# Kernel tuning notes

Measured on AMD Instinct MI355X. Metric: run time of the kernel, lower is better.

The kernel has to match this reference:

```python
import jax, jax.numpy as jnp
import numpy as np

B, CIN, H, W = 8, 256, 96, 96
EMB1, EMB2 = 256, 128
NCLS, NEG, NLAY = 80, 3, 3
SIGMA, BETA, NEG_SCOPE = 0.5, 0.3, 2.0


def setup_inputs() -> dict:
    key = jax.random.key(0)
    ks = jax.random.split(key, 8)
    s = 0.01
    return {
        "x": jax.random.normal(ks[0], (B, CIN, H, W), jnp.float32),
        "conv1_w": jax.random.normal(ks[1], (EMB1, CIN, 3, 3), jnp.float32) * s,
        "conv1_b": jnp.zeros((EMB1,), jnp.float32),
        "bn_gamma": jnp.ones((EMB1,), jnp.float32),
        "bn_beta": jnp.zeros((EMB1,), jnp.float32),
        "bn_mean": jnp.zeros((EMB1,), jnp.float32),
        "bn_var": jnp.ones((EMB1,), jnp.float32),
        "conv2_w": jax.random.normal(ks[2], (EMB2, EMB1, 3, 3), jnp.float32) * s,
        "conv2_b": jnp.zeros((EMB2,), jnp.float32),
        "rep_w": jax.random.normal(ks[3], (NCLS * EMB2, 1), jnp.float32) * s,
        "rep_b": jax.random.normal(ks[4], (NCLS * EMB2,), jnp.float32) * s,
        "neg_w": jax.random.normal(ks[5], (NEG, NLAY, EMB2, EMB2), jnp.float32) * s,
        "neg_b": jnp.zeros((NEG, NLAY, EMB2), jnp.float32),
    }


def _conv3(x, w, b):
    # 3x3, stride 1, padding 1 (SAME)
    y = jax.lax.conv_general_dilated(
        x, w, window_strides=(1, 1), padding="SAME",
        dimension_numbers=("NCHW", "OIHW", "NCHW"))
    return y + b[None, :, None, None]


def _l2norm(v, axis):
    return v / jnp.maximum(jnp.linalg.norm(v, axis=axis, keepdims=True), 1e-12)


def reference(x, conv1_w, conv1_b, bn_gamma, bn_beta, bn_mean, bn_var,
              conv2_w, conv2_b, rep_w, rep_b, neg_w, neg_b):
    # --- emb_module: Conv-BN-Conv, then L2 normalize channels ---
    h = _conv3(x, conv1_w, conv1_b)
    scale = bn_gamma / jnp.sqrt(bn_var + 1e-5)
    h = (h - bn_mean[None, :, None, None]) * scale[None, :, None, None] + bn_beta[None, :, None, None]
    emb = _conv3(h, conv2_w, conv2_b)          # [B, E, H, W]
    emb = _l2norm(emb, axis=1)

    # --- positive prototypes: rep_fc(1.0) -> [C, 1, E], normalized ---
    reps = (rep_w[:, 0] + rep_b).reshape(NCLS, 1, EMB2)
    reps = _l2norm(reps, axis=2)               # [C, 1, E]
    r = reps[:, 0]                              # [C, E]

    # --- negative prototypes: 3 MPCs (Linear-ReLU-Linear-ReLU-Linear) ---
    def mpc(Ws, bs):                            # Ws [NLAY,E,E], bs [NLAY,E]
        hh = r
        for i in range(NLAY):
            hh = hh @ Ws[i].T + bs[i]
            if i < NLAY - 1:
                hh = jax.nn.relu(hh)
        return hh                               # [C, E]
    reps_neg = jax.vmap(mpc)(neg_w, neg_b)      # [NEG, C, E]
    reps_neg = jnp.transpose(reps_neg, (1, 0, 2))  # [C, NEG, E]
    reps_neg = _l2norm(reps_neg, axis=2)

    # --- L2 distances; both sides unit-norm so ||e-r||^2 = 2 - 2 e.r ---
    dot = jnp.einsum("behw,cme->bcmhw", emb, reps)       # [B,C,1,H,W]
    distances = jnp.sqrt(jnp.maximum(2.0 - 2.0 * dot, 0.0))
    dot_n = jnp.einsum("behw,cme->bcmhw", emb, reps_neg)  # [B,C,NEG,H,W]
    distances_neg = jnp.sqrt(jnp.maximum(2.0 - 2.0 * dot_n, 0.0))

    inv2s2 = 1.0 / (2.0 * SIGMA ** 2)
    probs_neg = jnp.exp(-distances_neg ** 2 * inv2s2)
    cls_score_neg = probs_neg.max(axis=2)                 # [B,C,H,W]
    probs_ori = jnp.exp(-distances ** 2 * inv2s2).max(axis=2)

    min_neg = distances_neg.min(axis=2, keepdims=True)    # [B,C,1,H,W]
    shifted = distances + BETA * jax.nn.relu(NEG_SCOPE - min_neg)
    probs = jnp.exp(-shifted ** 2 * inv2s2)
    cls_score = probs.max(axis=2)                         # [B,C,H,W]

    # forward_single applies inverse_sigmoid to cls_score
    eps = 1e-5
    cs = jnp.clip(cls_score, 0.0, 1.0)
    cls_score = jnp.log(jnp.clip(cs, eps, None) / jnp.clip(1.0 - cs, eps, None))

    return (cls_score, cls_score_neg, distances, distances_neg, probs_ori)
```

## Files before the change

kernel.cpp:

```cpp
#include <hip/hip_runtime.h>
#include <cstddef>
#include <cstdint>

constexpr int Bz = 8, CIN = 256, Hh = 96, Ww = 96;
constexpr int EMB1 = 256, EMB2 = 128, NCLS = 80;
constexpr int HP = 98;
constexpr size_t PIX = (size_t)Hh * Ww;
constexpr size_t XP_ELEMS = (size_t)Bz * HP * HP * CIN;

constexpr size_t O0 = 0;
constexpr size_t O1 = (size_t)Bz * NCLS * PIX;
constexpr size_t O2 = 2 * O1;
constexpr size_t O3 = 3 * O1;
constexpr size_t O4 = 6 * O1;

typedef short bf16x8 __attribute__((ext_vector_type(8)));
typedef float f32x4 __attribute__((ext_vector_type(4)));

__device__ inline unsigned short f2bf(float f) {
  union { float f; unsigned int u; } v; v.f = f;
  unsigned int r = v.u + 0x7fffu + ((v.u >> 16) & 1u);
  return (unsigned short)(r >> 16);
}

#define GLD16(gp, lp)                                              \
  __builtin_amdgcn_global_load_lds(                                \
      (__attribute__((address_space(1))) void*)((void*)(gp)),      \
      (__attribute__((address_space(3))) void*)(lp), 16, 0, 0)

__global__ __launch_bounds__(256) void pad_x_kernel(const float* __restrict__ x,
                                                    unsigned short* __restrict__ xp) {
  __shared__ float tile[32][257];
  const int b = blockIdx.z, y = blockIdx.y, x0 = blockIdx.x * 32;
  const int t = threadIdx.x;
  const int px = t & 31, cg = t >> 5;
  const float* src = x + (((size_t)b * CIN) * Hh + y) * Ww + x0 + px;
#pragma unroll 4
  for (int c = cg; c < CIN; c += 8)
    tile[px][c] = src[(size_t)c * Hh * Ww];
  __syncthreads();
  unsigned short* orow =
      xp + (((size_t)b * HP + y + 1) * HP + (x0 + 1)) * 256 + t;
#pragma unroll 4
  for (int p = 0; p < 32; ++p)
    orow[(size_t)p * 256] = f2bf(tile[p][t]);
}

__global__ __launch_bounds__(256) void prep_w_kernel(
    const float* __restrict__ w1, const float* __restrict__ w2,
    const float* __restrict__ c1b, const float* __restrict__ g,
    const float* __restrict__ be, const float* __restrict__ mu,
    const float* __restrict__ var, unsigned short* __restrict__ wt1,
    unsigned short* __restrict__ wt2, float* __restrict__ bns,
    float* __restrict__ bno) {
  const int idx = blockIdx.x * 256 + threadIdx.x;
  if (idx < 9 * 256 * 256) {
    const int ic = idx & 255, oc = (idx >> 8) & 255, tap = idx >> 16;
    wt1[idx] = f2bf(w1[((size_t)(oc * 256 + ic)) * 9 + tap]);
  }
  if (idx < 9 * 128 * 256) {
    const int ic = idx & 255, oc = (idx >> 8) & 127, tap = idx >> 15;
    wt2[idx] = f2bf(w2[((size_t)(oc * 256 + ic)) * 9 + tap]);
  }
  if (idx < 256) {
    const float s = g[idx] * rsqrtf(var[idx] + 1e-5f);
    bns[idx] = s;
    bno[idx] = (c1b[idx] - mu[idx]) * s + be[idx];
  }
}

__global__ __launch_bounds__(128) void rep_norm_kernel(const float* __restrict__ rw,
                                                       const float* __restrict__ rb,
                                                       float* __restrict__ r,
                                                       unsigned short* __restrict__ Rb) {
  __shared__ float red[2];
  const int c = blockIdx.x, t = threadIdx.x;
  const float v = rw[c * 128 + t] + rb[c * 128 + t];
  float s = v * v;
  for (int msk = 1; msk < 64; msk <<= 1) s += __shfl_xor(s, msk, 64);
  if ((t & 63) == 0) red[t >> 6] = s;
  __syncthreads();
  const float ss = red[0] + red[1];
  const float rn = 1.f / fmaxf(sqrtf(ss), 1e-12f);
  r[c * 128 + t] = v * rn;
  Rb[(size_t)(c * 4) * 128 + t] = f2bf(v * rn);
}

__global__ __launch_bounds__(128) void mlp_neg_kernel(const float* __restrict__ r,
                                                      const float* __restrict__ W,
                                                      const float* __restrict__ bb,
                                                      unsigned short* __restrict__ Rb) {
  __shared__ float h0[128], h1[128];
  __shared__ float red[2];
  const int c = blockIdx.x, ng = blockIdx.y, t = threadIdx.x;
  h0[t] = r[c * 128 + t];
  __syncthreads();
  float s = 0.f;
  for (int lay = 0; lay < 3; ++lay) {
    const float* hin = (lay & 1) ? h1 : h0;
    float* hout = (lay & 1) ? h0 : h1;
    const float* wr = W + (((size_t)ng * 3 + lay) * 128 + t) * 128;
    s = bb[(ng * 3 + lay) * 128 + t];
    for (int e = 0; e < 128; ++e) s += wr[e] * hin[e];
    if (lay < 2) hout[t] = fmaxf(s, 0.f);
    __syncthreads();
  }
  float q = s * s;
  for (int msk = 1; msk < 64; msk <<= 1) q += __shfl_xor(q, msk, 64);
  if ((t & 63) == 0) red[t >> 6] = q;
  __syncthreads();
  const float ss = red[0] + red[1];
  const float rn = 1.f / fmaxf(sqrtf(ss), 1e-12f);
  Rb[((size_t)(c * 4) + 1 + ng) * 128 + t] = f2bf(s * rn);
}

template <int OC, bool BN>
__device__ __forceinline__ void conv3x3_body(
    const unsigned short* __restrict__ in, const unsigned short* __restrict__ wt,
    const float* __restrict__ e0, const float* __restrict__ e1,
    unsigned short* __restrict__ out16) {
  __shared__ unsigned short smA[2][128 * 32];
  __shared__ unsigned short smB[2][128 * 32];
  __shared__ float nrm[128][2];
  const int tile = blockIdx.x;
  const int oc0 = blockIdx.y * 128;
  const int b = blockIdx.z;
  const int ty = (tile / 6) * 8, tx = (tile % 6) * 16;
  const int t = threadIdx.x;
  const int lane = t & 63, w = t >> 6;
  const int wm = w & 1, wn = w >> 1;
  const int quad = lane >> 4, col = lane & 15;
  const int chl = (lane & 3) * 8;

  int rowA[2], colA[2];
  size_t bB0[2];
#pragma unroll
  for (int i = 0; i < 2; ++i) {
    const int px = (w * 2 + i) * 16 + (lane >> 2);
    rowA[i] = ty + (px >> 4);
    colA[i] = tx + (px & 15);
    const int ocB = oc0 + (w * 2 + i) * 16 + (lane >> 2);
    bB0[i] = (size_t)ocB * 256 + chl;
  }

  f32x4 acc[4][4];
#pragma unroll
  for (int mt = 0; mt < 4; ++mt)
#pragma unroll
    for (int nt = 0; nt < 4; ++nt) acc[mt][nt] = {0.f, 0.f, 0.f, 0.f};

  auto mk = [&](int tap, const unsigned short*& A0, const unsigned short*& A1,
                const unsigned short*& B0, const unsigned short*& B1) {
    const int ky = tap / 3, kx = tap % 3;
    A0 = in + (((size_t)b * HP + rowA[0] + ky) * HP + colA[0] + kx) * 256 + chl;
    A1 = in + (((size_t)b * HP + rowA[1] + ky) * HP + colA[1] + kx) * 256 + chl;
    B0 = wt + (size_t)tap * (OC * 256) + bB0[0];
    B1 = wt + (size_t)tap * (OC * 256) + bB0[1];
  };
  auto stage = [&](const unsigned short* A0, const unsigned short* A1,
                   const unsigned short* B0, const unsigned short* B1,
                   int ch, int buf) {
    GLD16(A0 + ch, (char*)smA[buf] + (w * 2 + 0) * 1024);
    GLD16(A1 + ch, (char*)smA[buf] + (w * 2 + 1) * 1024);
    GLD16(B0 + ch, (char*)smB[buf] + (w * 2 + 0) * 1024);
    GLD16(B1 + ch, (char*)smB[buf] + (w * 2 + 1) * 1024);
  };
  auto compute = [&](int buf) {
    bf16x8 af[4], bf[4];
#pragma unroll
    for (int mt = 0; mt < 4; ++mt)
      af[mt] = *(const bf16x8*)((const char*)smA[buf] +
                                (wm * 64 + mt * 16 + col) * 64 + quad * 16);
#pragma unroll
    for (int nt = 0; nt < 4; ++nt)
      bf[nt] = *(const bf16x8*)((const char*)smB[buf] +
                                (wn * 64 + nt * 16 + col) * 64 + quad * 16);
#pragma unroll
    for (int mt = 0; mt < 4; ++mt)
#pragma unroll
      for (int nt = 0; nt < 4; ++nt)
        acc[mt][nt] = __builtin_amdgcn_mfma_f32_16x16x32_bf16(
            af[mt], bf[nt], acc[mt][nt], 0, 0, 0);
  };

  const unsigned short *a0, *a1, *b0, *b1;
  mk(0, a0, a1, b0, b1);
  const unsigned short *a0n = a0, *a1n = a1, *b0n = b0, *b1n = b1;
  stage(a0, a1, b0, b1, 0, 0);
  __syncthreads();

  for (int tap = 0; tap < 9; ++tap) {
    if (tap < 8) mk(tap + 1, a0n, a1n, b0n, b1n);
#pragma unroll
    for (int cp = 0; cp < 4; ++cp) {
      const int c0 = cp * 64;
      stage(a0, a1, b0, b1, c0 + 32, 1);
      compute(0);
      __syncthreads();
      if (cp < 3)
        stage(a0, a1, b0, b1, c0 + 64, 0);
      else if (tap < 8)
        stage(a0n, a1n, b0n, b1n, 0, 0);
      compute(1);
      __syncthreads();
    }
    a0 = a0n; a1 = a1n; b0 = b0n; b1 = b1n;
  }

  float sc[4], of[4];
#pragma unroll
  for (int nt = 0; nt < 4; ++nt) {
    const int oc = oc0 + wn * 64 + nt * 16 + col;
    sc[nt] = e0[oc];
    of[nt] = BN ? e1[oc] : 0.f;
  }
  if (BN) {
#pragma unroll
    for (int mt = 0; mt < 4; ++mt)
#pragma unroll
      for (int r = 0; r < 4; ++r) {
        const int px = wm * 64 + mt * 16 + quad * 4 + r;
        const int y = ty + (px >> 4), x = tx + (px & 15);
        unsigned short* rowp =
            out16 + (((size_t)b * HP + y + 1) * HP + x + 1) * 256 + oc0 + wn * 64 + col;
#pragma unroll
        for (int nt = 0; nt < 4; ++nt)
          rowp[nt * 16] = f2bf(acc[mt][nt][r] * sc[nt] + of[nt]);
      }
  } else {
    float part[4][4];
#pragma unroll
    for (int mt = 0; mt < 4; ++mt)
#pragma unroll
      for (int r = 0; r < 4; ++r) {
        float s = 0.f;
#pragma unroll
        for (int nt = 0; nt < 4; ++nt) {
          const float v = acc[mt][nt][r] + sc[nt];
          s += v * v;
        }
        part[mt][r] = s;
      }
#pragma unroll
    for (int msk = 1; msk < 16; msk <<= 1)
#pragma unroll
      for (int mt = 0; mt < 4; ++mt)
#pragma unroll
        for (int r = 0; r < 4; ++r)
          part[mt][r] += __shfl_xor(part[mt][r], msk, 64);
    if (col == 0) {
#pragma unroll
      for (int mt = 0; mt < 4; ++mt)
#pragma unroll
        for (int r = 0; r < 4; ++r)
          nrm[wm * 64 + mt * 16 + quad * 4 + r][wn] = part[mt][r];
    }
    __syncthreads();
#pragma unroll
    for (int mt = 0; mt < 4; ++mt)
#pragma unroll
      for (int r = 0; r < 4; ++r) {
        const int px = wm * 64 + mt * 16 + quad * 4 + r;
        const int y = ty + (px >> 4), x = tx + (px & 15);
        const float nn = nrm[px][0] + nrm[px][1];
        const float rn = 1.f / fmaxf(sqrtf(nn), 1e-12f);
        unsigned short* rowp =
            out16 + (((size_t)b * Hh + y) * Ww + x) * 128 + wn * 64 + col;
#pragma unroll
        for (int nt = 0; nt < 4; ++nt)
          rowp[nt * 16] = f2bf((acc[mt][nt][r] + sc[nt]) * rn);
      }
  }
}

__global__ __launch_bounds__(256) void conv1_mfma(
    const unsigned short* __restrict__ in, const unsigned short* __restrict__ wt,
    const float* __restrict__ e0, const float* __restrict__ e1,
    unsigned short* __restrict__ out16) {
  conv3x3_body<256, true>(in, wt, e0, e1, out16);
}
__global__ __launch_bounds__(256) void conv2_mfma(
    const unsigned short* __restrict__ in, const unsigned short* __restrict__ wt,
    const float* __restrict__ e0, const float* __restrict__ e1,
    unsigned short* __restrict__ out16) {
  conv3x3_body<128, false>(in, wt, e0, e1, out16);
}

__device__ inline void xpose4(float& r0, float& r1, float& r2, float& r3,
                              int lane) {
  const int b1 = (lane >> 1) & 1, b0 = lane & 1;
  float s0 = b1 ? r0 : r2;
  float s1 = b1 ? r1 : r3;
  s0 = __shfl_xor(s0, 2, 64);
  s1 = __shfl_xor(s1, 2, 64);
  if (b1) { r0 = s0; r1 = s1; } else { r2 = s0; r3 = s1; }
  float t0 = b0 ? r0 : r1;
  float t1 = b0 ? r2 : r3;
  t0 = __shfl_xor(t0, 1, 64);
  t1 = __shfl_xor(t1, 1, 64);
  if (b0) { r0 = t0; r2 = t1; } else { r1 = t0; r3 = t1; }
}

__global__ __launch_bounds__(256) void score_mfma(
    const unsigned short* __restrict__ embb, const unsigned short* __restrict__ Rb,
    float* __restrict__ out) {
  const int px0 = blockIdx.x * 64;
  const int b = blockIdx.y;
  const int t = threadIdx.x;
  const int lane = t & 63, w = t >> 6;
  const int quad = lane >> 4, col = lane & 15;
  const int n0 = w * 80;
  const unsigned short* Abase = embb + ((size_t)b * PIX + px0) * 128;

  f32x4 acc[4][5];
#pragma unroll
  for (int mt = 0; mt < 4; ++mt)
#pragma unroll
    for (int nt = 0; nt < 5; ++nt) acc[mt][nt] = {0.f, 0.f, 0.f, 0.f};

#pragma unroll
  for (int ks = 0; ks < 4; ++ks) {
    bf16x8 bf[5], af[4];
#pragma unroll
    for (int nt = 0; nt < 5; ++nt)
      bf[nt] = *(const bf16x8*)(Rb + (size_t)(n0 + nt * 16 + col) * 128 +
                                ks * 32 + quad * 8);
#pragma unroll
    for (int mt = 0; mt < 4; ++mt)
      af[mt] = *(const bf16x8*)(Abase + (size_t)(mt * 16 + col) * 128 +
                                ks * 32 + quad * 8);
#pragma unroll
    for (int mt = 0; mt < 4; ++mt)
#pragma unroll
      for (int nt = 0; nt < 5; ++nt)
        acc[mt][nt] = __builtin_amdgcn_mfma_f32_16x16x32_bf16(
            af[mt], bf[nt], acc[mt][nt], 0, 0, 0);
  }

  const int j = lane & 3, kq = (lane >> 2) & 3;
#pragma unroll
  for (int mt = 0; mt < 4; ++mt) {
    const int px = px0 + mt * 16 + quad * 4 + j;
#pragma unroll
    for (int nt = 0; nt < 5; ++nt) {
      float v0 = acc[mt][nt][0], v1 = acc[mt][nt][1];
      float v2 = acc[mt][nt][2], v3 = acc[mt][nt][3];
      xpose4(v0, v1, v2, v3, lane);
      const int gc = w * 20 + nt * 4 + kq;
      const float d2p = fmaxf(2.f - 2.f * v0, 0.f);
      const float dist = sqrtf(d2p);
      const float q0 = fmaxf(2.f - 2.f * v1, 0.f);
      const float q1 = fmaxf(2.f - 2.f * v2, 0.f);
      const float q2 = fmaxf(2.f - 2.f * v3, 0.f);
      const float dn0 = sqrtf(q0), dn1 = sqrtf(q1), dn2 = sqrtf(q2);
      const float pn = __expf(-2.f * fminf(q0, fminf(q1, q2)));
      const float pori = __expf(-2.f * d2p);
      const float minn = fminf(dn0, fminf(dn1, dn2));
      const float shifted = dist + 0.3f * fmaxf(2.0f - minn, 0.f);
      const float p = __expf(-2.f * shifted * shifted);
      const float clsv = __logf(fmaxf(p, 1e-5f) / fmaxf(1.f - p, 1e-5f));
      const size_t bc = ((size_t)b * NCLS + gc) * PIX + px;
      out[O0 + bc] = clsv;
      out[O1 + bc] = pn;
      out[O2 + bc] = dist;
      out[O4 + bc] = pori;
      const size_t b3 = (((size_t)b * NCLS + gc) * 3) * PIX + px;
      out[O3 + b3] = dn0;
      out[O3 + b3 + PIX] = dn1;
      out[O3 + b3 + 2 * PIX] = dn2;
    }
  }
}

extern "C" void kernel_launch(void* const* d_in, const int* in_sizes, int n_in,
                              void* d_out, int out_size, void* d_ws,
                              size_t ws_size, hipStream_t stream) {
  const float* x = (const float*)d_in[0];
  const float* w1 = (const float*)d_in[1];
  const float* c1b = (const float*)d_in[2];
  const float* g = (const float*)d_in[3];
  const float* be = (const float*)d_in[4];
  const float* mu = (const float*)d_in[5];
  const float* var = (const float*)d_in[6];
  const float* w2 = (const float*)d_in[7];
  const float* c2b = (const float*)d_in[8];
  const float* rw = (const float*)d_in[9];
  const float* rb = (const float*)d_in[10];
  const float* nw = (const float*)d_in[11];
  const float* nb = (const float*)d_in[12];
  float* out = (float*)d_out;

  unsigned short* xp = (unsigned short*)d_ws;
  unsigned short* hp = xp + XP_ELEMS;
  unsigned short* wt1 = hp + XP_ELEMS;
  unsigned short* wt2 = wt1 + 589824;
  float* bns = (float*)(wt2 + 294912);
  float* bno = bns + 256;
  float* rpv = bno + 256;
  unsigned short* Rb = (unsigned short*)(rpv + 10240);
  unsigned short* embb = xp;

  hipMemsetAsync(xp, 0, XP_ELEMS * sizeof(unsigned short), stream);
  hipMemsetAsync(hp, 0, XP_ELEMS * sizeof(unsigned short), stream);
  pad_x_kernel<<<dim3(3, Hh, Bz), 256, 0, stream>>>(x, xp);
  prep_w_kernel<<<2304, 256, 0, stream>>>(w1, w2, c1b, g, be, mu, var, wt1, wt2,
                                          bns, bno);
  rep_norm_kernel<<<NCLS, 128, 0, stream>>>(rw, rb, rpv, Rb);
  mlp_neg_kernel<<<dim3(NCLS, 3), 128, 0, stream>>>(rpv, nw, nb, Rb);
  conv1_mfma<<<dim3(72, 2, Bz), 256, 0, stream>>>(xp, wt1, bns, bno, hp);
  conv2_mfma<<<dim3(72, 1, Bz), 256, 0, stream>>>(hp, wt2, c2b, nullptr, embb);
  score_mfma<<<dim3(144, Bz), 256, 0, stream>>>(embb, Rb, out);
}
```

Baseline: 564.6 us.

## Load conv MFMA operands directly from global memory instead of LDS staging

Removes the double-buffered LDS staging (global_load_lds plus barriers) in the 3x3 conv implicit GEMM, so each wave loads its bf16 A and B fragments straight from global memory into registers, with wave-uniform base offsets taken via readfirstlane. This drops the barrier synchronisation and LDS traffic. In exchange, tiles that were shared through LDS are now loaded separately by each wave that needs them, and there is no explicit prefetch to hide global latency, so the kernel relies on L1/L2 hits and occupancy.

```diff
diff --git a/kernel.cpp b/kernel.cpp
--- a/kernel.cpp
+++ b/kernel.cpp
@@ -22,11 +22,6 @@
   unsigned int r = v.u + 0x7fffu + ((v.u >> 16) & 1u);
   return (unsigned short)(r >> 16);
 }
-
-#define GLD16(gp, lp)                                              \
-  __builtin_amdgcn_global_load_lds(                                \
-      (__attribute__((address_space(1))) void*)((void*)(gp)),      \
-      (__attribute__((address_space(3))) void*)(lp), 16, 0, 0)
 
 __global__ __launch_bounds__(256) void pad_x_kernel(const float* __restrict__ x,
                                                     unsigned short* __restrict__ xp) {
@@ -119,8 +114,6 @@
     const unsigned short* __restrict__ in, const unsigned short* __restrict__ wt,
     const float* __restrict__ e0, const float* __restrict__ e1,
     unsigned short* __restrict__ out16) {
-  __shared__ unsigned short smA[2][128 * 32];
-  __shared__ unsigned short smB[2][128 * 32];
   __shared__ float nrm[128][2];
   const int tile = blockIdx.x;
   const int oc0 = blockIdx.y * 128;
@@ -130,18 +123,8 @@
   const int lane = t & 63, w = t >> 6;
   const int wm = w & 1, wn = w >> 1;
   const int quad = lane >> 4, col = lane & 15;
-  const int chl = (lane & 3) * 8;
-
-  int rowA[2], colA[2];
-  size_t bB0[2];
-#pragma unroll
-  for (int i = 0; i < 2; ++i) {
-    const int px = (w * 2 + i) * 16 + (lane >> 2);
-    rowA[i] = ty + (px >> 4);
-    colA[i] = tx + (px & 15);
-    const int ocB = oc0 + (w * 2 + i) * 16 + (lane >> 2);
-    bB0[i] = (size_t)ocB * 256 + chl;
-  }
+
+  const int laneO = col * 256 + quad * 8;
 
   f32x4 acc[4][4];
 #pragma unroll
@@ -149,62 +132,34 @@
 #pragma unroll
     for (int nt = 0; nt < 4; ++nt) acc[mt][nt] = {0.f, 0.f, 0.f, 0.f};
 
-  auto mk = [&](int tap, const unsigned short*& A0, const unsigned short*& A1,
-                const unsigned short*& B0, const unsigned short*& B1) {
+  for (int tap = 0; tap < 9; ++tap) {
     const int ky = tap / 3, kx = tap % 3;
-    A0 = in + (((size_t)b * HP + rowA[0] + ky) * HP + colA[0] + kx) * 256 + chl;
-    A1 = in + (((size_t)b * HP + rowA[1] + ky) * HP + colA[1] + kx) * 256 + chl;
-    B0 = wt + (size_t)tap * (OC * 256) + bB0[0];
-    B1 = wt + (size_t)tap * (OC * 256) + bB0[1];
-  };
-  auto stage = [&](const unsigned short* A0, const unsigned short* A1,
-                   const unsigned short* B0, const unsigned short* B1,
-                   int ch, int buf) {
-    GLD16(A0 + ch, (char*)smA[buf] + (w * 2 + 0) * 1024);
-    GLD16(A1 + ch, (char*)smA[buf] + (w * 2 + 1) * 1024);
-    GLD16(B0 + ch, (char*)smB[buf] + (w * 2 + 0) * 1024);
-    GLD16(B1 + ch, (char*)smB[buf] + (w * 2 + 1) * 1024);
-  };
-  auto compute = [&](int buf) {
-    bf16x8 af[4], bf[4];
-#pragma unroll
-    for (int mt = 0; mt < 4; ++mt)
-      af[mt] = *(const bf16x8*)((const char*)smA[buf] +
-                                (wm * 64 + mt * 16 + col) * 64 + quad * 16);
+    int uA[4], uB[4];
+#pragma unroll
+    for (int mt = 0; mt < 4; ++mt)
+      uA[mt] = __builtin_amdgcn_readfirstlane(
+          (int)((((b * HP) + ty + wm * 4 + mt + ky) * HP + tx + kx) * 256));
 #pragma unroll
     for (int nt = 0; nt < 4; ++nt)
-      bf[nt] = *(const bf16x8*)((const char*)smB[buf] +
-                                (wn * 64 + nt * 16 + col) * 64 + quad * 16);
-#pragma unroll
-    for (int mt = 0; mt < 4; ++mt)
+      uB[nt] = __builtin_amdgcn_readfirstlane(
+          (tap * OC + oc0 + wn * 64 + nt * 16) * 256);
+#pragma unroll
+    for (int c8 = 0; c8 < 8; ++c8) {
+      const int ch0 = c8 * 32;
+      bf16x8 af[4], bf[4];
+#pragma unroll
+      for (int mt = 0; mt < 4; ++mt)
+        af[mt] = *(const bf16x8*)(in + uA[mt] + laneO + ch0);
 #pragma unroll
       for (int nt = 0; nt < 4; ++nt)
-        acc[mt][nt] = __builtin_amdgcn_mfma_f32_16x16x32_bf16(
-            af[mt], bf[nt], acc[mt][nt], 0, 0, 0);
-  };
-
-  const unsigned short *a0, *a1, *b0, *b1;
-  mk(0, a0, a1, b0, b1);
-  const unsigned short *a0n = a0, *a1n = a1, *b0n = b0, *b1n = b1;
-  stage(a0, a1, b0, b1, 0, 0);
-  __syncthreads();
-
-  for (int tap = 0; tap < 9; ++tap) {
-    if (tap < 8) mk(tap + 1, a0n, a1n, b0n, b1n);
-#pragma unroll
-    for (int cp = 0; cp < 4; ++cp) {
-      const int c0 = cp * 64;
-      stage(a0, a1, b0, b1, c0 + 32, 1);
-      compute(0);
-      __syncthreads();
-      if (cp < 3)
-        stage(a0, a1, b0, b1, c0 + 64, 0);
-      else if (tap < 8)
-        stage(a0n, a1n, b0n, b1n, 0, 0);
-      compute(1);
-      __syncthreads();
+        bf[nt] = *(const bf16x8*)(wt + uB[nt] + laneO + ch0);
+#pragma unroll
+      for (int mt = 0; mt < 4; ++mt)
+#pragma unroll
+        for (int nt = 0; nt < 4; ++nt)
+          acc[mt][nt] = __builtin_amdgcn_mfma_f32_16x16x32_bf16(
+              af[mt], bf[nt], acc[mt][nt], 0, 0, 0);
     }
-    a0 = a0n; a1 = a1n; b0 = b0n; b1 = b1n;
   }
 
   float sc[4], of[4];
```

Result: slower. 882.0 us (+56.2%).
